# Kernel optimization log

Hardware: AMD Instinct MI355X
Metric: run time of the kernel (lower is better)

The kernel has to match this reference:

```python
import jax, jax.numpy as jnp
import numpy as np

N_RAYS = 16384
NS = 128
FD = 32
HID = 64
GS = 128
NEAR = 0.1
FAR = 100.0  # unused by the original forward body
EARLY_TERM = 1e-4


def mip360_contract(c):
    # inf-norm scene contraction (Mip-NeRF 360); safe denom avoids NaN grads in untaken branch
    norm = jnp.max(jnp.abs(c), axis=-1, keepdims=True)
    ns = jnp.maximum(norm, 1.0)
    return jnp.where(norm <= 1.0, c, (2.0 - 1.0 / ns) * c / ns) / 2.0


def grid_sample_trilinear(grid, coords):
    # torch.nn.functional.grid_sample 5D, mode='bilinear', padding='zeros', align_corners=False
    # grid: [D,H,W]; coords[...,0]=x->W, coords[...,1]=y->H, coords[...,2]=z->D, in [-1,1]
    D, H, W = grid.shape
    x = ((coords[..., 0] + 1.0) * W - 1.0) * 0.5
    y = ((coords[..., 1] + 1.0) * H - 1.0) * 0.5
    z = ((coords[..., 2] + 1.0) * D - 1.0) * 0.5
    x0 = jnp.floor(x); y0 = jnp.floor(y); z0 = jnp.floor(z)
    fx = x - x0; fy = y - y0; fz = z - z0
    x0 = x0.astype(jnp.int32); y0 = y0.astype(jnp.int32); z0 = z0.astype(jnp.int32)

    def corner(zi, yi, xi):
        valid = ((zi >= 0) & (zi < D) & (yi >= 0) & (yi < H) & (xi >= 0) & (xi < W))
        v = grid[jnp.clip(zi, 0, D - 1), jnp.clip(yi, 0, H - 1), jnp.clip(xi, 0, W - 1)]
        return v * valid.astype(grid.dtype)

    out = (corner(z0, y0, x0) * (1 - fz) * (1 - fy) * (1 - fx)
           + corner(z0, y0, x0 + 1) * (1 - fz) * (1 - fy) * fx
           + corner(z0, y0 + 1, x0) * (1 - fz) * fy * (1 - fx)
           + corner(z0, y0 + 1, x0 + 1) * (1 - fz) * fy * fx
           + corner(z0 + 1, y0, x0) * fz * (1 - fy) * (1 - fx)
           + corner(z0 + 1, y0, x0 + 1) * fz * (1 - fy) * fx
           + corner(z0 + 1, y0 + 1, x0) * fz * fy * (1 - fx)
           + corner(z0 + 1, y0 + 1, x0 + 1) * fz * fy * fx)
    return out


def setup_inputs() -> dict:
    key = jax.random.key(0)
    ks = jax.random.split(key, 9)
    rays_o = jax.random.normal(ks[0], (N_RAYS, 3), jnp.float32) * 0.1
    rd = jax.random.normal(ks[1], (N_RAYS, 3), jnp.float32)
    rays_d = rd / jnp.linalg.norm(rd, axis=-1, keepdims=True)
    grid = (jax.random.uniform(ks[2], (GS, GS, GS)) > 0.3).astype(jnp.float32)

    def lin(k, fin, fout):
        return jax.random.normal(k, (fin, fout), jnp.float32) * (1.0 / np.sqrt(fin))

    return {
        "rays_o": rays_o, "rays_d": rays_d, "grid": grid,
        "W1": lin(ks[3], 3, HID), "b1": jnp.zeros(HID, jnp.float32),
        "W2": lin(ks[4], HID, FD), "b2": jnp.zeros(FD, jnp.float32),
        "Ws": lin(ks[5], FD, 1), "bs": jnp.zeros(1, jnp.float32),
        "Wr1": lin(ks[6], FD + 3, HID), "br1": jnp.zeros(HID, jnp.float32),
        "Wr2": lin(ks[7], HID, 3), "br2": jnp.zeros(3, jnp.float32),
        "n_samples": NS,
    }


def reference(rays_o, rays_d, grid, W1, b1, W2, b2, Ws, bs, Wr1, br1, Wr2, br2, n_samples):
    n = rays_o.shape[0]
    half = n_samples // 2
    t_close = jnp.linspace(NEAR, NEAR + 1.0, half, dtype=jnp.float32)
    t_far = jnp.exp(jnp.arange(half, dtype=jnp.float32) * np.float32(np.log(1.0 + 1.0 / 256.0))) * (NEAR + 1.0)
    t_values = jnp.concatenate([t_close, t_far])
    distances = t_values[1:] - t_values[:-1]          # [S]
    t_values = t_values[:-1]                          # [S], S = n_samples - 1 (eval mode: no jitter)

    samples = rays_o[:, None, :] + rays_d[:, None, :] * t_values[None, :, None]   # [n,S,3]
    sc = mip360_contract(samples)
    occ = grid_sample_trilinear(grid, sc)             # [n,S]
    mask = occ > 0.0                                  # .bool() of sampled occupancy
    maskf = mask.astype(sc.dtype)

    # feature MLP; zero where unmasked (torch scatters into a zeros buffer)
    feat = jax.nn.relu(sc @ W1 + b1) @ W2 + b2        # [n,S,FD]
    feat = feat * maskf[..., None]
    sigma = jax.nn.softplus(feat @ Ws + bs)[..., 0] * maskf   # [n,S]

    alpha_log = -sigma * distances[None, :]
    trans = jnp.exp(jnp.cumsum(alpha_log, axis=1))
    trans = jnp.concatenate([jnp.ones((n, 1), sc.dtype), trans[:, :-1]], axis=1)
    alpha = 1.0 - jnp.exp(alpha_log)
    weights = trans * alpha                           # [n,S]

    mask2 = mask & (weights > EARLY_TERM)
    dirs = jnp.broadcast_to(rays_d[:, None, :], samples.shape)
    h = jax.nn.relu(jnp.concatenate([feat, dirs], axis=-1) @ Wr1 + br1)
    rgb = jax.nn.sigmoid(h @ Wr2 + br2) * weights[..., None]
    rgb = rgb * mask2[..., None].astype(sc.dtype)
    return rgb.sum(axis=1)                            # [n,3]
```

## Files before the change

kernel.cpp:

```cpp
#include <hip/hip_runtime.h>
#include <math.h>

#define HID 64
#define FD 32
#define ROWB 144

typedef __fp16 f16x8 __attribute__((ext_vector_type(8)));
typedef __fp16 f16x2v __attribute__((ext_vector_type(2)));
typedef float  f32x4 __attribute__((ext_vector_type(4)));
typedef unsigned int u32x4 __attribute__((ext_vector_type(4)));
typedef unsigned int u32x2 __attribute__((ext_vector_type(2)));

__device__ __forceinline__ unsigned int pk2(float a, float b) {
    auto v = __builtin_amdgcn_cvt_pkrtz(a, b);
    return __builtin_bit_cast(unsigned int, v);
}
__device__ __forceinline__ unsigned int pkadd(unsigned int a, unsigned int b) {
    f16x2v x = __builtin_bit_cast(f16x2v, a), y = __builtin_bit_cast(f16x2v, b);
    f16x2v r = x + y;
    return __builtin_bit_cast(unsigned int, r);
}
__device__ __forceinline__ unsigned int pkmax0(unsigned int a) {
    f16x2v x = __builtin_bit_cast(f16x2v, a);
    f16x2v z = {(__fp16)0.f, (__fp16)0.f};
    f16x2v r = __builtin_elementwise_max(x, z);
    return __builtin_bit_cast(unsigned int, r);
}
__device__ __forceinline__ f32x4 mfma16(f16x8 a, f16x8 b, f32x4 c) {
    return __builtin_amdgcn_mfma_f32_16x16x32_f16(a, b, c, 0, 0, 0);
}

__device__ __forceinline__ float t_of(int i) {
    #pragma clang fp contract(off)
    if (i < 64) {
        if (i == 63) return 1.1f;
        return (float)(0.1 + (double)i * (1.0 / 63.0));
    }
    const float LOGC = 0.0038986404159402954f;
    float arg = (float)(i - 64) * LOGC;
    return (float)exp((double)arg) * 1.1f;
}

__global__ void prep(const float* __restrict__ W1, const float* __restrict__ b1,
                     const float* __restrict__ W2, const float* __restrict__ b2,
                     const float* __restrict__ Ws, const float* __restrict__ bs,
                     const float* __restrict__ Wr1, const float* __restrict__ br1,
                     const float* __restrict__ Wr2,
                     unsigned char* __restrict__ wsb) {
    __shared__ float wv[64];
    const int t = threadIdx.x;
    if (t < 64) {
        float acc = 0.f;
        for (int k = 0; k < FD; ++k) acc = fmaf(W2[t*FD+k], Ws[k], acc);
        wv[t] = acc;
    }
    __syncthreads();
    float* b2e = (float*)(wsb + 20480);
    unsigned int* fpk  = (unsigned int*)(wsb + 20672);
    unsigned int* r1pk = (unsigned int*)(wsb + 20736);
    float* ttab = (float*)(wsb + 20864);
    float* dtab = (float*)(wsb + 21376);
    if (t < 48) {
        float v = 0.f;
        if (t < 32) v = b2[t];
        else if (t == 32) {
            float c = bs[0];
            for (int k = 0; k < FD; ++k) c = fmaf(b2[k], Ws[k], c);
            v = c;
        }
        b2e[t] = v;
    }
    if (t >= 64 && t < 192) { int s = t - 64; ttab[s] = t_of(s); dtab[s] = t_of(s+1) - t_of(s); }
    if (t >= 192 && t < 208) {
        int e = t - 192, mt = e >> 3, g = (e >> 1) & 3, p = e & 1;
        int row = 16*mt + 4*g + 2*p;
        fpk[e] = pk2(b2[row], b2[row+1]);
    }
    if (t >= 208 && t < 240) {
        int e = t - 208, mt = e >> 3, g = (e >> 1) & 3, p = e & 1;
        int row = 16*mt + 4*g + 2*p;
        r1pk[e] = pk2(br1[row], br1[row+1]);
    }
    const int f = t >> 6, lane = t & 63;
    const int c15 = lane & 15, g = lane >> 4;
    f16x8 o;
    #pragma unroll
    for (int j = 0; j < 8; ++j) {
        float v = 0.f;
        if (f < 6) {
            int mt = f >> 1, kc = f & 1, row = 16*mt + c15;
            int kg = 32*kc + 8*g + j;
            v = (row < 32) ? W2[kg*FD + row] : ((row == 32) ? wv[kg] : 0.f);
        } else if (f < 14) {
            int ff = f - 6, mt = ff >> 1, kc = ff & 1, row = 16*mt + c15;
            int kg = 32*kc + 8*g + j;
            v = (kg < FD+3) ? Wr1[kg*HID + row] : 0.f;
        } else {
            int kc = f - 14, row = c15;
            int kg = 32*kc + 8*g + j;
            v = (row < 3) ? Wr2[kg*3 + row] : 0.f;
        }
        o[j] = (__fp16)v;
    }
    *(f16x8*)(wsb + (f*64 + lane)*16) = o;
    if (f < 4) {
        f16x8 o2;
        #pragma unroll
        for (int j = 0; j < 8; ++j) {
            int row = 16*f + c15, k = 8*g + j;
            float v = 0.f;
            if (k < 3)       v = W1[k*HID + row];
            else if (k < 6)  v = W1[(k-3)*HID + row];
            else if (k == 6) v = b1[row];
            o2[j] = (__fp16)v;
        }
        *(f16x8*)(wsb + ((16+f)*64 + lane)*16) = o2;
    }
}

__device__ __forceinline__ bool gv(const float* __restrict__ g, int zi, int yi, int xi) {
    bool ok = ((unsigned)zi < 128u) & ((unsigned)yi < 128u) & ((unsigned)xi < 128u);
    int zc = min(max(zi, 0), 127);
    int yc = min(max(yi, 0), 127);
    int xc = min(max(xi, 0), 127);
    float v = g[(((zc << 7) + yc) << 7) + xc];
    return ok & (v > 0.5f);
}

__global__ __launch_bounds__(256) void nerf_render(
    const float* __restrict__ rays_o, const float* __restrict__ rays_d,
    const float* __restrict__ grid,  const float* __restrict__ br2,
    const unsigned char* __restrict__ wsb,
    float* __restrict__ out)
{
    __shared__ unsigned char lds[40960] __attribute__((aligned(16)));
    const int lane = threadIdx.x & 63;
    const int wid  = threadIdx.x >> 6;
    const int ray  = (blockIdx.x << 2) + wid;
    const int c15 = lane & 15, g = lane >> 4;

    unsigned char* ldsH = lds + wid*10240;
    float* ldsSig = (float*)(lds + wid*10240 + 9216);
    float* ldsRgb = (float*)(lds + wid*10240 + 9472);

    const f16x8* AF = (const f16x8*)wsb;
    const float* b2e = (const float*)(wsb + 20480);
    const unsigned int* fpk  = (const unsigned int*)(wsb + 20672);
    const unsigned int* r1pk = (const unsigned int*)(wsb + 20736);
    const float* ttab = (const float*)(wsb + 20864);
    const float* dtab = (const float*)(wsb + 21376);

    const float ox = rays_o[ray*3+0], oy = rays_o[ray*3+1], oz = rays_o[ray*3+2];
    const float dx = rays_d[ray*3+0], dy = rays_d[ray*3+1], dz = rays_d[ray*3+2];

    const float b2e32 = b2e[32];
    unsigned int fpkv[2][2], r1pkv[4][2];
    #pragma unroll
    for (int mt = 0; mt < 2; ++mt) { fpkv[mt][0] = fpk[mt*8+g*2]; fpkv[mt][1] = fpk[mt*8+g*2+1]; }
    #pragma unroll
    for (int mt = 0; mt < 4; ++mt) { r1pkv[mt][0] = r1pk[mt*8+g*2]; r1pkv[mt][1] = r1pk[mt*8+g*2+1]; }
    const unsigned int p3c = pk2(1.f, 0.f);

    f16x8 bd;
    #pragma unroll
    for (int j = 0; j < 8; ++j) bd[j] = (__fp16)0.f;
    if (g == 0) { bd[0] = (__fp16)dx; bd[1] = (__fp16)dy; bd[2] = (__fp16)dz; }

    float rr = 0.f, rg = 0.f, rb = 0.f;
    float carry = 0.f;

    #pragma unroll 1
    for (int chunk = 0; chunk < 2; ++chunk) {
        const int s  = (chunk << 6) + lane;
        const bool vs = (s < 127);
        const float tv = ttab[s];
        const float dist = dtab[s];

        float cx, cy, cz, fx, fy, fz;
        int x0, y0, z0;
        {
            #pragma clang fp contract(off)
            float px = ox + dx * tv;
            float py = oy + dy * tv;
            float pz = oz + dz * tv;
            float nrm = fmaxf(fabsf(px), fmaxf(fabsf(py), fabsf(pz)));
            if (nrm <= 1.0f) { cx = px; cy = py; cz = pz; }
            else {
                float t2 = 2.0f - 1.0f / nrm;
                cx = (t2 * px) / nrm; cy = (t2 * py) / nrm; cz = (t2 * pz) / nrm;
            }
            cx = cx * 0.5f; cy = cy * 0.5f; cz = cz * 0.5f;
            float gx = ((cx + 1.0f) * 128.0f - 1.0f) * 0.5f;
            float gy = ((cy + 1.0f) * 128.0f - 1.0f) * 0.5f;
            float gz = ((cz + 1.0f) * 128.0f - 1.0f) * 0.5f;
            float xf = floorf(gx), yf = floorf(gy), zf = floorf(gz);
            fx = gx - xf; fy = gy - yf; fz = gz - zf;
            x0 = (int)xf; y0 = (int)yf; z0 = (int)zf;
        }
        const bool fxp = fx > 0.f, fyp = fy > 0.f, fzp = fz > 0.f;
        bool m = gv(grid, z0,   y0,   x0)
             | (fxp             & gv(grid, z0,   y0,   x0+1))
             | (fyp             & gv(grid, z0,   y0+1, x0))
             | (fyp & fxp       & gv(grid, z0,   y0+1, x0+1))
             | (fzp             & gv(grid, z0+1, y0,   x0))
             | (fzp & fxp       & gv(grid, z0+1, y0,   x0+1))
             | (fzp & fyp       & gv(grid, z0+1, y0+1, x0))
             | (fzp & fyp & fxp & gv(grid, z0+1, y0+1, x0+1));
        m = m & vs;

        if (__ballot(m)) {
            float xh = (float)(__fp16)cx, yh = (float)(__fp16)cy, zh = (float)(__fp16)cz;
            unsigned int q0 = pk2(xh, yh);
            unsigned int q1 = pk2(zh, cx - xh);
            unsigned int q2 = pk2(cy - yh, cz - zh);

            f16x8 bl1[4];
            #pragma unroll
            for (int nt = 0; nt < 4; ++nt) {
                int ad = (16*nt + c15) << 2;
                u32x4 bw;
                bw[0] = (unsigned int)__builtin_amdgcn_ds_bpermute(ad, (int)q0);
                bw[1] = (unsigned int)__builtin_amdgcn_ds_bpermute(ad, (int)q1);
                bw[2] = (unsigned int)__builtin_amdgcn_ds_bpermute(ad, (int)q2);
                bw[3] = p3c;
                bl1[nt] = __builtin_bit_cast(f16x8, bw);
            }
            #pragma unroll
            for (int mt = 0; mt < 4; ++mt) {
                f16x8 a = AF[(16+mt)*64 + lane];
                #pragma unroll
                for (int nt = 0; nt < 4; ++nt) {
                    f32x4 z = {0.f,0.f,0.f,0.f};
                    z = mfma16(a, bl1[nt], z);
                    u32x2 ww;
                    ww[0] = pkmax0(pk2(z[0], z[1]));
                    ww[1] = pkmax0(pk2(z[2], z[3]));
                    *(u32x2*)(ldsH + (16*nt + c15)*ROWB + 32*mt + 8*g) = ww;
                }
            }
            f16x8 bh[4][2];
            #pragma unroll
            for (int nt = 0; nt < 4; ++nt)
                #pragma unroll
                for (int kc = 0; kc < 2; ++kc)
                    bh[nt][kc] = *(const f16x8*)(ldsH + (16*nt + c15)*ROWB + 64*kc + 16*g);

            #pragma unroll
            for (int mt = 0; mt < 3; ++mt) {
                f16x8 a0 = AF[(mt*2+0)*64 + lane];
                f16x8 a1 = AF[(mt*2+1)*64 + lane];
                f32x4 acc[4];
                #pragma unroll
                for (int nt = 0; nt < 4; ++nt) { f32x4 z = {0.f,0.f,0.f,0.f}; acc[nt] = z; }
                #pragma unroll
                for (int nt = 0; nt < 4; ++nt) acc[nt] = mfma16(a0, bh[nt][0], acc[nt]);
                #pragma unroll
                for (int nt = 0; nt < 4; ++nt) acc[nt] = mfma16(a1, bh[nt][1], acc[nt]);
                if (mt < 2) {
                    #pragma unroll
                    for (int nt = 0; nt < 4; ++nt) {
                        u32x2 ww;
                        ww[0] = pkadd(pk2(acc[nt][0], acc[nt][1]), fpkv[mt][0]);
                        ww[1] = pkadd(pk2(acc[nt][2], acc[nt][3]), fpkv[mt][1]);
                        *(u32x2*)(ldsH + (16*nt + c15)*ROWB + 32*mt + 8*g) = ww;
                    }
                } else if (g == 0) {
                    #pragma unroll
                    for (int nt = 0; nt < 4; ++nt)
                        ldsSig[16*nt + c15] = acc[nt][0] + b2e32;
                }
            }
            const float spre = ldsSig[lane];
            const float sp = fmaxf(spre, 0.f) + log1pf(expf(-fabsf(spre)));
            const float sigma = m ? sp : 0.f;
            const float al = -sigma * dist;

            float xs = al;
            #pragma unroll
            for (int d = 1; d < 64; d <<= 1) {
                float y = __shfl_up(xs, (unsigned)d, 64);
                if (lane >= d) xs += y;
            }
            const float total = __shfl(xs, 63, 64);
            const float trans = expf(carry + (xs - al));
            const float alpha = 1.0f - expf(al);
            const float w = trans * alpha;
            carry += total;

            const bool m2 = m & (w > 1e-4f);
            if (__ballot(m2)) {
                f16x8 bf[4];
                #pragma unroll
                for (int nt = 0; nt < 4; ++nt)
                    bf[nt] = *(const f16x8*)(ldsH + (16*nt + c15)*ROWB + 16*g);
                #pragma unroll
                for (int mt = 0; mt < 4; ++mt) {
                    f16x8 a0 = AF[(6 + mt*2 + 0)*64 + lane];
                    f16x8 a1 = AF[(6 + mt*2 + 1)*64 + lane];
                    f32x4 acc[4];
                    #pragma unroll
                    for (int nt = 0; nt < 4; ++nt) { f32x4 z = {0.f,0.f,0.f,0.f}; acc[nt] = z; }
                    #pragma unroll
                    for (int nt = 0; nt < 4; ++nt) acc[nt] = mfma16(a0, bf[nt], acc[nt]);
                    #pragma unroll
                    for (int nt = 0; nt < 4; ++nt) acc[nt] = mfma16(a1, bd, acc[nt]);
                    #pragma unroll
                    for (int nt = 0; nt < 4; ++nt) {
                        u32x2 ww;
                        ww[0] = pkmax0(pkadd(pk2(acc[nt][0], acc[nt][1]), r1pkv[mt][0]));
                        ww[1] = pkmax0(pkadd(pk2(acc[nt][2], acc[nt][3]), r1pkv[mt][1]));
                        *(u32x2*)(ldsH + (16*nt + c15)*ROWB + 32*mt + 8*g) = ww;
                    }
                }
                f16x8 a0 = AF[14*64 + lane];
                f16x8 a1 = AF[15*64 + lane];
                f32x4 accr[4];
                #pragma unroll
                for (int nt = 0; nt < 4; ++nt) {
                    f16x8 q0c = *(const f16x8*)(ldsH + (16*nt + c15)*ROWB + 16*g);
                    f16x8 q1c = *(const f16x8*)(ldsH + (16*nt + c15)*ROWB + 64 + 16*g);
                    f32x4 z = {0.f,0.f,0.f,0.f};
                    z = mfma16(a0, q0c, z);
                    z = mfma16(a1, q1c, z);
                    accr[nt] = z;
                }
                if (g == 0) {
                    const float c0 = br2[0], c1 = br2[1], c2 = br2[2];
                    #pragma unroll
                    for (int nt = 0; nt < 4; ++nt) {
                        float* rp = ldsRgb + (16*nt + c15)*3;
                        rp[0] = accr[nt][0] + c0;
                        rp[1] = accr[nt][1] + c1;
                        rp[2] = accr[nt][2] + c2;
                    }
                }
                const float* rp = ldsRgb + lane*3;
                const float l0 = rp[0], l1 = rp[1], l2 = rp[2];
                const float wm = m2 ? w : 0.f;
                rr = fmaf(1.f/(1.f + expf(-l0)), wm, rr);
                rg = fmaf(1.f/(1.f + expf(-l1)), wm, rg);
                rb = fmaf(1.f/(1.f + expf(-l2)), wm, rb);
            }
            if (chunk == 0 && expf(carry) <= 5e-5f) break;
        }
    }

    #pragma unroll
    for (int d = 32; d > 0; d >>= 1) {
        rr += __shfl_xor(rr, d, 64);
        rg += __shfl_xor(rg, d, 64);
        rb += __shfl_xor(rb, d, 64);
    }
    if (lane == 0) {
        out[ray*3+0] = rr;
        out[ray*3+1] = rg;
        out[ray*3+2] = rb;
    }
}

extern "C" void kernel_launch(void* const* d_in, const int* in_sizes, int n_in,
                              void* d_out, int out_size, void* d_ws, size_t ws_size,
                              hipStream_t stream) {
    const float* rays_o = (const float*)d_in[0];
    const float* rays_d = (const float*)d_in[1];
    const float* grid   = (const float*)d_in[2];
    const float* W1  = (const float*)d_in[3];
    const float* b1  = (const float*)d_in[4];
    const float* W2  = (const float*)d_in[5];
    const float* b2  = (const float*)d_in[6];
    const float* Ws  = (const float*)d_in[7];
    const float* bs  = (const float*)d_in[8];
    const float* Wr1 = (const float*)d_in[9];
    const float* br1 = (const float*)d_in[10];
    const float* Wr2 = (const float*)d_in[11];
    const float* br2 = (const float*)d_in[12];
    float* out = (float*)d_out;
    unsigned char* ws = (unsigned char*)d_ws;

    prep<<<dim3(1), dim3(1024), 0, stream>>>(W1, b1, W2, b2, Ws, bs, Wr1, br1, Wr2, ws);
    nerf_render<<<dim3(16384/4), dim3(256), 0, stream>>>(
        rays_o, rays_d, grid, br2, ws, out);
}
```

Measured before the change: 175.8 us.

## Use one-wave blocks with XOR-swizzled LDS, shuffle-based sigma/rgb exchange, and setprio

Each ray now runs in its own 64-thread block, with a smaller LDS footprint per block and launch bounds requesting more waves per SIMD. The padded 144-byte LDS rows become 128-byte rows with an XOR swizzle to avoid bank conflicts. Sigma and RGB logits move between lanes through wave shuffles instead of LDS round-trips, and the MFMA sections are wrapped in s_setprio. The early-exit test compares the log-transmittance directly instead of calling expf. The aim is higher occupancy and less LDS traffic, at the cost of more shuffles and smaller blocks to schedule.

```diff
diff --git a/kernel.cpp b/kernel.cpp
--- a/kernel.cpp
+++ b/kernel.cpp
@@ -3,7 +3,7 @@
 
 #define HID 64
 #define FD 32
-#define ROWB 144
+#define ROWP 128
 
 typedef __fp16 f16x8 __attribute__((ext_vector_type(8)));
 typedef __fp16 f16x2v __attribute__((ext_vector_type(2)));
@@ -127,21 +127,17 @@
     return ok & (v > 0.5f);
 }
 
-__global__ __launch_bounds__(256) void nerf_render(
+__global__ __launch_bounds__(64, 5) void nerf_render(
     const float* __restrict__ rays_o, const float* __restrict__ rays_d,
     const float* __restrict__ grid,  const float* __restrict__ br2,
     const unsigned char* __restrict__ wsb,
     float* __restrict__ out)
 {
-    __shared__ unsigned char lds[40960] __attribute__((aligned(16)));
-    const int lane = threadIdx.x & 63;
-    const int wid  = threadIdx.x >> 6;
-    const int ray  = (blockIdx.x << 2) + wid;
+    __shared__ unsigned char ldsH[8192] __attribute__((aligned(16)));
+    const int lane = threadIdx.x;
+    const int ray  = blockIdx.x;
     const int c15 = lane & 15, g = lane >> 4;
-
-    unsigned char* ldsH = lds + wid*10240;
-    float* ldsSig = (float*)(lds + wid*10240 + 9216);
-    float* ldsRgb = (float*)(lds + wid*10240 + 9472);
+    const int swc = (c15 & 7) << 4;
 
     const f16x8* AF = (const f16x8*)wsb;
     const float* b2e = (const float*)(wsb + 20480);
@@ -160,6 +156,7 @@
     #pragma unroll
     for (int mt = 0; mt < 4; ++mt) { r1pkv[mt][0] = r1pk[mt*8+g*2]; r1pkv[mt][1] = r1pk[mt*8+g*2+1]; }
     const unsigned int p3c = pk2(1.f, 0.f);
+    const float c0b = br2[0], c1b = br2[1], c2b = br2[2];
 
     f16x8 bd;
     #pragma unroll
@@ -225,6 +222,7 @@
                 bw[3] = p3c;
                 bl1[nt] = __builtin_bit_cast(f16x8, bw);
             }
+            __builtin_amdgcn_s_setprio(1);
             #pragma unroll
             for (int mt = 0; mt < 4; ++mt) {
                 f16x8 a = AF[(16+mt)*64 + lane];
@@ -235,16 +233,19 @@
                     u32x2 ww;
                     ww[0] = pkmax0(pk2(z[0], z[1]));
                     ww[1] = pkmax0(pk2(z[2], z[3]));
-                    *(u32x2*)(ldsH + (16*nt + c15)*ROWB + 32*mt + 8*g) = ww;
+                    *(u32x2*)(ldsH + (16*nt + c15)*ROWP + ((32*mt + 8*g) ^ swc)) = ww;
                 }
             }
+            __builtin_amdgcn_s_setprio(0);
             f16x8 bh[4][2];
             #pragma unroll
             for (int nt = 0; nt < 4; ++nt)
                 #pragma unroll
                 for (int kc = 0; kc < 2; ++kc)
-                    bh[nt][kc] = *(const f16x8*)(ldsH + (16*nt + c15)*ROWB + 64*kc + 16*g);
-
+                    bh[nt][kc] = *(const f16x8*)(ldsH + (16*nt + c15)*ROWP + ((64*kc + 16*g) ^ swc));
+
+            float sq[4];
+            __builtin_amdgcn_s_setprio(1);
             #pragma unroll
             for (int mt = 0; mt < 3; ++mt) {
                 f16x8 a0 = AF[(mt*2+0)*64 + lane];
@@ -262,15 +263,19 @@
                         u32x2 ww;
                         ww[0] = pkadd(pk2(acc[nt][0], acc[nt][1]), fpkv[mt][0]);
                         ww[1] = pkadd(pk2(acc[nt][2], acc[nt][3]), fpkv[mt][1]);
-                        *(u32x2*)(ldsH + (16*nt + c15)*ROWB + 32*mt + 8*g) = ww;
+                        *(u32x2*)(ldsH + (16*nt + c15)*ROWP + ((32*mt + 8*g) ^ swc)) = ww;
                     }
-                } else if (g == 0) {
-                    #pragma unroll
-                    for (int nt = 0; nt < 4; ++nt)
-                        ldsSig[16*nt + c15] = acc[nt][0] + b2e32;
+                } else {
+                    #pragma unroll
+                    for (int nt = 0; nt < 4; ++nt) sq[nt] = acc[nt][0] + b2e32;
                 }
             }
-            const float spre = ldsSig[lane];
+            __builtin_amdgcn_s_setprio(0);
+            const float sg0 = __shfl(sq[0], c15, 64);
+            const float sg1 = __shfl(sq[1], c15, 64);
+            const float sg2 = __shfl(sq[2], c15, 64);
+            const float sg3 = __shfl(sq[3], c15, 64);
+            const float spre = (g < 2) ? (g == 0 ? sg0 : sg1) : (g == 2 ? sg2 : sg3);
             const float sp = fmaxf(spre, 0.f) + log1pf(expf(-fabsf(spre)));
             const float sigma = m ? sp : 0.f;
             const float al = -sigma * dist;
@@ -292,7 +297,8 @@
                 f16x8 bf[4];
                 #pragma unroll
                 for (int nt = 0; nt < 4; ++nt)
-                    bf[nt] = *(const f16x8*)(ldsH + (16*nt + c15)*ROWB + 16*g);
+                    bf[nt] = *(const f16x8*)(ldsH + (16*nt + c15)*ROWP + ((16*g) ^ swc));
+                __builtin_amdgcn_s_setprio(1);
                 #pragma unroll
                 for (int mt = 0; mt < 4; ++mt) {
                     f16x8 a0 = AF[(6 + mt*2 + 0)*64 + lane];
@@ -309,7 +315,7 @@
                         u32x2 ww;
                         ww[0] = pkmax0(pkadd(pk2(acc[nt][0], acc[nt][1]), r1pkv[mt][0]));
                         ww[1] = pkmax0(pkadd(pk2(acc[nt][2], acc[nt][3]), r1pkv[mt][1]));
-                        *(u32x2*)(ldsH + (16*nt + c15)*ROWB + 32*mt + 8*g) = ww;
+                        *(u32x2*)(ldsH + (16*nt + c15)*ROWP + ((32*mt + 8*g) ^ swc)) = ww;
                     }
                 }
                 f16x8 a0 = AF[14*64 + lane];
@@ -317,31 +323,31 @@
                 f32x4 accr[4];
                 #pragma unroll
                 for (int nt = 0; nt < 4; ++nt) {
-                    f16x8 q0c = *(const f16x8*)(ldsH + (16*nt + c15)*ROWB + 16*g);
-                    f16x8 q1c = *(const f16x8*)(ldsH + (16*nt + c15)*ROWB + 64 + 16*g);
+                    f16x8 q0c = *(const f16x8*)(ldsH + (16*nt + c15)*ROWP + ((16*g) ^ swc));
+                    f16x8 q1c = *(const f16x8*)(ldsH + (16*nt + c15)*ROWP + ((64 + 16*g) ^ swc));
                     f32x4 z = {0.f,0.f,0.f,0.f};
                     z = mfma16(a0, q0c, z);
                     z = mfma16(a1, q1c, z);
                     accr[nt] = z;
                 }
-                if (g == 0) {
-                    const float c0 = br2[0], c1 = br2[1], c2 = br2[2];
-                    #pragma unroll
-                    for (int nt = 0; nt < 4; ++nt) {
-                        float* rp = ldsRgb + (16*nt + c15)*3;
-                        rp[0] = accr[nt][0] + c0;
-                        rp[1] = accr[nt][1] + c1;
-                        rp[2] = accr[nt][2] + c2;
-                    }
-                }
-                const float* rp = ldsRgb + lane*3;
-                const float l0 = rp[0], l1 = rp[1], l2 = rp[2];
+                __builtin_amdgcn_s_setprio(0);
+                float t0, t1, t2, t3, l0, l1, l2;
+                t0 = __shfl(accr[0][0], c15, 64); t1 = __shfl(accr[1][0], c15, 64);
+                t2 = __shfl(accr[2][0], c15, 64); t3 = __shfl(accr[3][0], c15, 64);
+                l0 = ((g < 2) ? (g == 0 ? t0 : t1) : (g == 2 ? t2 : t3)) + c0b;
+                t0 = __shfl(accr[0][1], c15, 64); t1 = __shfl(accr[1][1], c15, 64);
+                t2 = __shfl(accr[2][1], c15, 64); t3 = __shfl(accr[3][1], c15, 64);
+                l1 = ((g < 2) ? (g == 0 ? t0 : t1) : (g == 2 ? t2 : t3)) + c1b;
+                t0 = __shfl(accr[0][2], c15, 64); t1 = __shfl(accr[1][2], c15, 64);
+                t2 = __shfl(accr[2][2], c15, 64); t3 = __shfl(accr[3][2], c15, 64);
+                l2 = ((g < 2) ? (g == 0 ? t0 : t1) : (g == 2 ? t2 : t3)) + c2b;
+
                 const float wm = m2 ? w : 0.f;
                 rr = fmaf(1.f/(1.f + expf(-l0)), wm, rr);
                 rg = fmaf(1.f/(1.f + expf(-l1)), wm, rg);
                 rb = fmaf(1.f/(1.f + expf(-l2)), wm, rb);
             }
-            if (chunk == 0 && expf(carry) <= 5e-5f) break;
+            if (chunk == 0 && carry <= -9.9034875f) break;
         }
     }
 
@@ -378,6 +384,6 @@
     unsigned char* ws = (unsigned char*)d_ws;
 
     prep<<<dim3(1), dim3(1024), 0, stream>>>(W1, b1, W2, b2, Ws, bs, Wr1, br1, Wr2, ws);
-    nerf_render<<<dim3(16384/4), dim3(256), 0, stream>>>(
+    nerf_render<<<dim3(16384), dim3(64), 0, stream>>>(
         rays_o, rays_d, grid, br2, ws, out);
 }
```

New measurement: 208.6 us. +18.6%, slower.
